# Performance work log

Hardware: AMD Instinct MI355X
Metric: run time of the kernel (lower is better)

## Reference

```python
import jax, jax.numpy as jnp
import numpy as np

N = 100000
E = 1600000
D = 128  # embedding_dim
H = 128  # hidden_channels


def setup_inputs() -> dict:
    key = jax.random.key(0)
    ks = jax.random.split(key, 8)
    x = jax.random.normal(ks[0], (N, D), dtype=jnp.float32)
    edge_index = jax.random.randint(ks[1], (2, E), 0, N, dtype=jnp.int64)
    s = 1.0 / np.sqrt(D)
    W1l = jax.random.uniform(ks[2], (H, D), minval=-s, maxval=s, dtype=jnp.float32)
    W1r = jax.random.uniform(ks[3], (H, D), minval=-s, maxval=s, dtype=jnp.float32)
    b1 = jnp.zeros((H,), dtype=jnp.float32)
    s2 = 1.0 / np.sqrt(H)
    W2l = jax.random.uniform(ks[4], (H, H), minval=-s2, maxval=s2, dtype=jnp.float32)
    W2r = jax.random.uniform(ks[5], (H, H), minval=-s2, maxval=s2, dtype=jnp.float32)
    b2 = jnp.zeros((H,), dtype=jnp.float32)
    return {"x": x, "edge_index": edge_index, "W1l": W1l, "b1": b1, "W1r": W1r,
            "W2l": W2l, "b2": b2, "W2r": W2r}


def _sage_conv(h, src, dst, Wl, b, Wr, n_nodes):
    # mean aggregation of source-node features onto target nodes
    msg = h[src]                                             # [E, F] gather
    agg = jax.ops.segment_sum(msg, dst, num_segments=n_nodes)  # [N, F]
    deg = jax.ops.segment_sum(jnp.ones((src.shape[0],), h.dtype), dst,
                              num_segments=n_nodes)
    mean = agg / jnp.maximum(deg, 1.0)[:, None]
    return mean @ Wl.T + b + h @ Wr.T                        # lin_l(agg) + lin_r(x)


def reference(x, edge_index, W1l, b1, W1r, W2l, b2, W2r):
    src, dst = edge_index[0], edge_index[1]
    n = x.shape[0]
    x1 = jax.nn.relu(_sage_conv(x, src, dst, W1l, b1, W1r, n))
    x2 = jax.nn.relu(_sage_conv(x1, src, dst, W2l, b2, W2r, n))
    return jnp.concatenate((x1[:, :, None], x2[:, :, None]), axis=2)  # [N, H, 2]
```

## Files before the change

kernel.cpp:

```cpp
#include <hip/hip_runtime.h>

typedef unsigned char u8;
typedef unsigned short u16;
typedef unsigned int u32;
typedef unsigned long long u64;
typedef short bf16x8 __attribute__((ext_vector_type(8)));
typedef float f32x4 __attribute__((ext_vector_type(4)));
typedef float f32x2 __attribute__((ext_vector_type(2)));

#define NSB 32
#define MAXW 26
#define CAPL 513
#define CAPW 3072
#define CAPQ 768
#define G1 512
#define CH2 16

static __device__ __forceinline__ float relu(float v) { return v > 0.f ? v : 0.f; }

static __device__ __forceinline__ u16 f2bf(float f) {
  u32 u = __float_as_uint(f);
  u32 r = (u + 0x7FFF + ((u >> 16) & 1)) >> 16;
  return (u16)r;
}
static __device__ __forceinline__ u32 pack2(float a, float b) {
  return (u32)f2bf(a) | ((u32)f2bf(b) << 16);
}

__global__ __launch_bounds__(256) void k_stage(
    const float* __restrict__ w1l, const float* __restrict__ w1r,
    const float* __restrict__ w2l, const float* __restrict__ w2r,
    u16* __restrict__ bfrag,
    const float* __restrict__ x, u16* __restrict__ xb, u8* __restrict__ x8,
    int total8,
    const int* __restrict__ dst, int* __restrict__ Hist1,
    int e, u32 magic, int perBlock, int gPrep, int gF2b) {
  __shared__ int h[NSB];
  int tid = threadIdx.x;
  int b = blockIdx.x;
  if (b < gPrep) {
    int i = b * 256 + tid;
    int ee = i & 7;
    int lane = (i >> 3) & 63;
    int jb = (i >> 9) & 7;
    int ks = (i >> 12) & 7;
    int m = i >> 15;
    int k = ks * 32 + (lane >> 4) * 8 + ee;
    int j = jb * 16 + (lane & 15);
    const float* wl = m ? w2l : w1l;
    const float* wr = m ? w2r : w1r;
    float v = (k < 128) ? wl[j * 128 + k] : wr[j * 128 + (k - 128)];
    bfrag[i] = f2bf(v);
  } else if (b < gPrep + gF2b) {
    int i = (b - gPrep) * 256 + tid;
    if (i < total8) {
      const float4* xp = (const float4*)x;
      float4 a = xp[i * 2];
      float4 bb = xp[i * 2 + 1];
      uint4 o;
      o.x = pack2(a.x, a.y);
      o.y = pack2(a.z, a.w);
      o.z = pack2(bb.x, bb.y);
      o.w = pack2(bb.z, bb.w);
      ((uint4*)xb)[i] = o;
      u32 lo = __builtin_amdgcn_cvt_pk_fp8_f32(a.x, a.y, 0u, false);
      lo = __builtin_amdgcn_cvt_pk_fp8_f32(a.z, a.w, lo, true);
      u32 hi = __builtin_amdgcn_cvt_pk_fp8_f32(bb.x, bb.y, 0u, false);
      hi = __builtin_amdgcn_cvt_pk_fp8_f32(bb.z, bb.w, hi, true);
      uint2 q = {lo, hi};
      ((uint2*)x8)[i] = q;
    }
  } else {
    int hb = b - gPrep - gF2b;
    if (tid < NSB) h[tid] = 0;
    __syncthreads();
    int start = hb * perBlock;
    int end = min(start + perBlock, e);
    for (int i = start + tid; i < end; i += 256) {
      int d = dst[i];
      int sb = (int)(((u64)(u32)d * magic) >> 32);
      atomicAdd(&h[sb], 1);
    }
    __syncthreads();
    if (tid < NSB) Hist1[hb * NSB + tid] = h[tid];
  }
}

__global__ __launch_bounds__(256) void k_offs1(const int* __restrict__ Hist1,
                                               int* __restrict__ Off1,
                                               int* __restrict__ binBase1,
                                               int* __restrict__ binCnt1) {
  __shared__ int tot[NSB], base[NSB];
  int tid = threadIdx.x, lane = tid & 63, wave = tid >> 6;
  for (int b = wave * 8; b < wave * 8 + 8; ++b) {
    int run = 0;
    for (int s = 0; s < G1; s += 64) {
      int v = Hist1[(s + lane) * NSB + b];
      int sum = v;
#pragma unroll
      for (int o = 1; o < 64; o <<= 1) sum += __shfl_xor(sum, o, 64);
      run += sum;
    }
    if (lane == 0) tot[b] = run;
  }
  __syncthreads();
  if (tid == 0) {
    int r = 0;
    for (int b = 0; b < NSB; ++b) {
      base[b] = r;
      binBase1[b] = r;
      binCnt1[b] = tot[b];
      r += tot[b];
    }
  }
  __syncthreads();
  for (int b = wave * 8; b < wave * 8 + 8; ++b) {
    int run = base[b];
    for (int s = 0; s < G1; s += 64) {
      int v = Hist1[(s + lane) * NSB + b];
      int incl = v;
#pragma unroll
      for (int o = 1; o < 64; o <<= 1) {
        int t = __shfl_up(incl, o, 64);
        if (lane >= o) incl += t;
      }
      Off1[(s + lane) * NSB + b] = run + incl - v;
      run += __shfl(incl, 63, 64);
    }
  }
}

__global__ __launch_bounds__(256) void k_scatA(const int* __restrict__ src,
                                               const int* __restrict__ dst,
                                               const int* __restrict__ Off1,
                                               u32* __restrict__ gbinA,
                                               int e, int sbn, u32 magic, int perBlock) {
  __shared__ u32 lbuf[NSB * CAPL];
  __shared__ int lcnt[NSB], myOff[NSB];
  int tid = threadIdx.x, lane = tid & 63, wave = tid >> 6;
  if (tid < NSB) {
    lcnt[tid] = 0;
    myOff[tid] = Off1[blockIdx.x * NSB + tid];
  }
  __syncthreads();
  int start = blockIdx.x * perBlock;
  int end = min(start + perBlock, e);
  for (int base = start; base < end; base += 2048) {
    int bend = min(base + 2048, end);
    for (int i = base + tid; i < bend; i += 256) {
      int d = dst[i];
      int s = src[i];
      int sb = (int)(((u64)(u32)d * magic) >> 32);
      int dl = d - sb * sbn;
      u32 w = (u32)s | ((u32)dl << 17);
      int pos = atomicAdd(&lcnt[sb], 1);
      if (pos < CAPL) lbuf[sb * CAPL + pos] = w;
      else gbinA[myOff[sb] + pos] = w;
    }
    __syncthreads();
    for (int b = wave; b < NSB; b += 4) {
      int cnt = lcnt[b];
      int staged = min(cnt, CAPL);
      int gp = myOff[b];
      for (int off = lane; off < staged; off += 64) gbinA[gp + off] = lbuf[b * CAPL + off];
      if (lane == 0) {
        myOff[b] = gp + cnt;
        lcnt[b] = 0;
      }
    }
    __syncthreads();
  }
}

__global__ __launch_bounds__(256) void k_hist2(const u32* __restrict__ gbinA,
                                               const int* __restrict__ binBase1,
                                               const int* __restrict__ binCnt1,
                                               int* __restrict__ Hist2) {
  __shared__ int h[MAXW];
  int tid = threadIdx.x;
  int sb = blockIdx.x >> 4, ch = blockIdx.x & (CH2 - 1);
  if (tid < MAXW) h[tid] = 0;
  __syncthreads();
  int b0 = binBase1[sb], cnt = binCnt1[sb];
  int per = (cnt + CH2 - 1) / CH2;
  int s = b0 + ch * per, e2 = min(s + per, b0 + cnt);
  for (int i = s + tid; i < e2; i += 256) {
    int wn = (int)(gbinA[i] >> 24);
    atomicAdd(&h[wn], 1);
  }
  __syncthreads();
  if (tid < MAXW) Hist2[blockIdx.x * MAXW + tid] = h[tid];
}

__global__ __launch_bounds__(512) void k_offs2(const int* __restrict__ Hist2,
                                               int* __restrict__ Off2,
                                               int* __restrict__ winBase,
                                               int* __restrict__ winCnt, int wins) {
  __shared__ int tot[NSB * MAXW], baseL[NSB * MAXW];
  int tid = threadIdx.x, lane = tid & 63;
  int nw = NSB * wins;
  for (int wi = tid; wi < nw; wi += 512) {
    int sb = wi / wins, wn = wi - sb * wins;
    int r = 0;
    for (int ch = 0; ch < CH2; ++ch) r += Hist2[(sb * CH2 + ch) * MAXW + wn];
    tot[wi] = r;
  }
  __syncthreads();
  if (tid < 64) {
    int run = 0;
    for (int s = 0; s < nw; s += 64) {
      int idx = s + lane;
      int v = (idx < nw) ? tot[idx] : 0;
      int incl = v;
#pragma unroll
      for (int o = 1; o < 64; o <<= 1) {
        int t = __shfl_up(incl, o, 64);
        if (lane >= o) incl += t;
      }
      if (idx < nw) {
        baseL[idx] = run + incl - v;
        winBase[idx] = run + incl - v;
        winCnt[idx] = v;
      }
      run += __shfl(incl, 63, 64);
    }
  }
  __syncthreads();
  for (int wi = tid; wi < nw; wi += 512) {
    int sb = wi / wins, wn = wi - sb * wins;
    int r = baseL[wi];
    for (int ch = 0; ch < CH2; ++ch) {
      Off2[(sb * CH2 + ch) * MAXW + wn] = r;
      r += Hist2[(sb * CH2 + ch) * MAXW + wn];
    }
  }
}

__global__ __launch_bounds__(256) void k_scatB(const u32* __restrict__ gbinA,
                                               const int* __restrict__ binBase1,
                                               const int* __restrict__ binCnt1,
                                               const int* __restrict__ Off2,
                                               u32* __restrict__ gbin2, int wins) {
  __shared__ u32 lbuf[MAXW * CAPL];
  __shared__ int lcnt[MAXW], myOff[MAXW];
  int tid = threadIdx.x, lane = tid & 63, wave = tid >> 6;
  int sb = blockIdx.x >> 4, ch = blockIdx.x & (CH2 - 1);
  if (tid < MAXW) {
    lcnt[tid] = 0;
    myOff[tid] = Off2[blockIdx.x * MAXW + tid];
  }
  __syncthreads();
  int b0 = binBase1[sb], cnt = binCnt1[sb];
  int per = (cnt + CH2 - 1) / CH2;
  int s = b0 + ch * per, e2 = min(s + per, b0 + cnt);
  for (int base = s; base < e2; base += 2048) {
    int bend = min(base + 2048, e2);
    for (int i = base + tid; i < bend; i += 256) {
      u32 w = gbinA[i];
      int wn = (int)(w >> 24);
      u32 w2 = w & 0x00FFFFFFu;
      int pos = atomicAdd(&lcnt[wn], 1);
      if (pos < CAPL) lbuf[wn * CAPL + pos] = w2;
      else gbin2[myOff[wn] + pos] = w2;
    }
    __syncthreads();
    for (int b = wave; b < wins; b += 4) {
      int c = lcnt[b];
      int staged = min(c, CAPL);
      int gp = myOff[b];
      for (int off = lane; off < staged; off += 64) gbin2[gp + off] = lbuf[b * CAPL + off];
      if (lane == 0) {
        myOff[b] = gp + c;
        lcnt[b] = 0;
      }
    }
    __syncthreads();
  }
}

__global__ __launch_bounds__(256) void k_sort3(const u32* __restrict__ gbin2,
                                               const int* __restrict__ winBase,
                                               const int* __restrict__ winCnt,
                                               u32* __restrict__ gbin3,
                                               int* __restrict__ winOffs) {
  __shared__ int cnt[128], offs[128], cur[128];
  int widx = blockIdx.x, tid = threadIdx.x;
  int wstart = winBase[widx];
  int wcnt = min(winCnt[widx], CAPW);
  if (tid < 128) cnt[tid] = 0;
  __syncthreads();
  for (int i = tid; i < wcnt; i += 256) atomicAdd(&cnt[gbin2[wstart + i] >> 17], 1);
  __syncthreads();
  if (tid < 64) {
    int lane = tid;
    int c0 = cnt[lane * 2], c1 = cnt[lane * 2 + 1];
    int p = c0 + c1, incl = p;
#pragma unroll
    for (int o = 1; o < 64; o <<= 1) {
      int t = __shfl_up(incl, o, 64);
      if (lane >= o) incl += t;
    }
    offs[lane * 2] = incl - p;
    offs[lane * 2 + 1] = incl - c1;
  }
  __syncthreads();
  if (tid < 128) {
    cur[tid] = offs[tid];
    winOffs[(size_t)widx * 128 + tid] = offs[tid];
  }
  __syncthreads();
  for (int i = tid; i < wcnt; i += 256) {
    u32 w = gbin2[wstart + i];
    int pos = atomicAdd(&cur[w >> 17], 1);
    gbin3[wstart + pos] = w & 0x1FFFFu;
  }
}

__global__ __launch_bounds__(256, 8) void k_agg(
    const u8* __restrict__ h8,
    const u32* __restrict__ gbin3,
    const int* __restrict__ winBase, const int* __restrict__ winCnt,
    const int* __restrict__ winOffs, u32* __restrict__ mean,
    int n, int sbn, int wins) {
  __shared__ u32 elist[CAPQ];
  __shared__ int offs[33];
  int tid = threadIdx.x, lane = tid & 63, wid = tid >> 6;
  int widx = blockIdx.x >> 2, quarter = blockIdx.x & 3;
  int sb = widx / wins, win = widx - sb * wins;
  int winNodeBase = sb * sbn + win * 128;
  int rowsTot = min(min(128, sbn - win * 128), n - winNodeBase);
  int rowsQ = min(max(rowsTot - quarter * 32, 0), 32);
  int nodeBase = winNodeBase + quarter * 32;
  int wstart = winBase[widx];
  int wcnt = min(winCnt[widx], CAPW);
  if (tid <= 32) {
    int r = quarter * 32 + tid;
    offs[tid] = (r >= 128) ? wcnt : min(winOffs[(size_t)widx * 128 + r], wcnt);
  }
  __syncthreads();
  int s0 = offs[0];
  int cnt = min(offs[32] - s0, CAPQ);
  for (int i = tid; i < cnt; i += 256) elist[i] = gbin3[wstart + s0 + i];
  __syncthreads();

  int grp = lane >> 4, l16 = lane & 15;
  const uint2* hp = (const uint2*)h8 + l16;
#pragma unroll 1
  for (int rp = 0; rp < 2; ++rp) {
    int r = wid * 8 + rp * 4 + grp;
    int s = offs[r] - s0;
    int c = min(offs[r + 1] - s0, cnt) - s;
    if (c < 0) c = 0;
    f32x2 A0 = {0.f, 0.f}, A1 = {0.f, 0.f}, A2 = {0.f, 0.f}, A3 = {0.f, 0.f};
    uint2 v0 = {0u, 0u}, v1 = {0u, 0u}, v2 = {0u, 0u}, v3 = {0u, 0u};
    if (0 < c) v0 = hp[(size_t)elist[s + 0] * 16];
    if (1 < c) v1 = hp[(size_t)elist[s + 1] * 16];
    if (2 < c) v2 = hp[(size_t)elist[s + 2] * 16];
    if (3 < c) v3 = hp[(size_t)elist[s + 3] * 16];
#pragma unroll 1
    for (int t = 4; t < c + 4; t += 4) {
      uint2 n0 = {0u, 0u}, n1 = {0u, 0u}, n2 = {0u, 0u}, n3 = {0u, 0u};
      if (t + 0 < c) n0 = hp[(size_t)elist[s + t + 0] * 16];
      if (t + 1 < c) n1 = hp[(size_t)elist[s + t + 1] * 16];
      if (t + 2 < c) n2 = hp[(size_t)elist[s + t + 2] * 16];
      if (t + 3 < c) n3 = hp[(size_t)elist[s + t + 3] * 16];
      A0 += __builtin_amdgcn_cvt_pk_f32_fp8(v0.x, false);
      A1 += __builtin_amdgcn_cvt_pk_f32_fp8(v0.x, true);
      A2 += __builtin_amdgcn_cvt_pk_f32_fp8(v0.y, false);
      A3 += __builtin_amdgcn_cvt_pk_f32_fp8(v0.y, true);
      A0 += __builtin_amdgcn_cvt_pk_f32_fp8(v1.x, false);
      A1 += __builtin_amdgcn_cvt_pk_f32_fp8(v1.x, true);
      A2 += __builtin_amdgcn_cvt_pk_f32_fp8(v1.y, false);
      A3 += __builtin_amdgcn_cvt_pk_f32_fp8(v1.y, true);
      A0 += __builtin_amdgcn_cvt_pk_f32_fp8(v2.x, false);
      A1 += __builtin_amdgcn_cvt_pk_f32_fp8(v2.x, true);
      A2 += __builtin_amdgcn_cvt_pk_f32_fp8(v2.y, false);
      A3 += __builtin_amdgcn_cvt_pk_f32_fp8(v2.y, true);
      A0 += __builtin_amdgcn_cvt_pk_f32_fp8(v3.x, false);
      A1 += __builtin_amdgcn_cvt_pk_f32_fp8(v3.x, true);
      A2 += __builtin_amdgcn_cvt_pk_f32_fp8(v3.y, false);
      A3 += __builtin_amdgcn_cvt_pk_f32_fp8(v3.y, true);
      v0 = n0; v1 = n1; v2 = n2; v3 = n3;
    }
    A0 += __builtin_amdgcn_cvt_pk_f32_fp8(v0.x, false);
    A1 += __builtin_amdgcn_cvt_pk_f32_fp8(v0.x, true);
    A2 += __builtin_amdgcn_cvt_pk_f32_fp8(v0.y, false);
    A3 += __builtin_amdgcn_cvt_pk_f32_fp8(v0.y, true);
    A0 += __builtin_amdgcn_cvt_pk_f32_fp8(v1.x, false);
    A1 += __builtin_amdgcn_cvt_pk_f32_fp8(v1.x, true);
    A2 += __builtin_amdgcn_cvt_pk_f32_fp8(v1.y, false);
    A3 += __builtin_amdgcn_cvt_pk_f32_fp8(v1.y, true);
    A0 += __builtin_amdgcn_cvt_pk_f32_fp8(v2.x, false);
    A1 += __builtin_amdgcn_cvt_pk_f32_fp8(v2.x, true);
    A2 += __builtin_amdgcn_cvt_pk_f32_fp8(v2.y, false);
    A3 += __builtin_amdgcn_cvt_pk_f32_fp8(v2.y, true);
    A0 += __builtin_amdgcn_cvt_pk_f32_fp8(v3.x, false);
    A1 += __builtin_amdgcn_cvt_pk_f32_fp8(v3.x, true);
    A2 += __builtin_amdgcn_cvt_pk_f32_fp8(v3.y, false);
    A3 += __builtin_amdgcn_cvt_pk_f32_fp8(v3.y, true);
    if (r < rowsQ) {
      float inv = 1.f / (float)(c > 0 ? c : 1);
      uint4 o;
      o.x = pack2(A0.x * inv, A0.y * inv);
      o.y = pack2(A1.x * inv, A1.y * inv);
      o.z = pack2(A2.x * inv, A2.y * inv);
      o.w = pack2(A3.x * inv, A3.y * inv);
      *(uint4*)(mean + (size_t)(nodeBase + r) * 64 + l16 * 4) = o;
    }
  }
}

template <int MODE>
__global__ __launch_bounds__(512) void k_gemm(
    const u32* __restrict__ Am, const u32* __restrict__ Ax,
    const u16* __restrict__ Bfrag, const float* __restrict__ bias,
    u16* __restrict__ x1out, u8* __restrict__ x8out,
    float* __restrict__ out, int n) {
  __shared__ u16 lA[128 * 256];

  int tid = threadIdx.x, lane = tid & 63, wid = tid >> 6;
  int l15 = lane & 15, lhi = lane >> 4;
  int wr = wid >> 1, wc = wid & 1;
  int r0 = blockIdx.x * 128;

#pragma unroll
  for (int it = 0; it < 8; ++it) {
    int i = tid + it * 512;
    int row = i >> 5, c = i & 31;
    int gr = r0 + row;
    uint4 v = {0u, 0u, 0u, 0u};
    if (gr < n)
      v = (c < 16) ? ((const uint4*)(Am + (size_t)gr * 64))[c]
                   : ((const uint4*)(Ax + (size_t)gr * 64))[c - 16];
    int byteoff = (row * 512 + c * 16) ^ ((row & 7) << 4);
    *(uint4*)((char*)lA + byteoff) = v;
  }

  float bs[4];
#pragma unroll
  for (int nj = 0; nj < 4; ++nj) bs[nj] = bias[wc * 64 + nj * 16 + l15];

  __syncthreads();

  f32x4 acc[2][4];
#pragma unroll
  for (int mi = 0; mi < 2; ++mi)
#pragma unroll
    for (int nj = 0; nj < 4; ++nj) acc[mi][nj] = (f32x4){0.f, 0.f, 0.f, 0.f};

#pragma unroll
  for (int ks = 0; ks < 8; ++ks) {
    bf16x8 af[2], bfr[4];
#pragma unroll
    for (int mi = 0; mi < 2; ++mi) {
      int row = wr * 32 + mi * 16 + l15;
      int byteoff = (row * 512 + ks * 64 + lhi * 16) ^ ((row & 7) << 4);
      af[mi] = *(const bf16x8*)((const char*)lA + byteoff);
    }
#pragma unroll
    for (int nj = 0; nj < 4; ++nj) {
      int jb = wc * 4 + nj;
      bfr[nj] = *(const bf16x8*)(Bfrag + ((ks * 8 + jb) * 64 + lane) * 8);
    }
#pragma unroll
    for (int mi = 0; mi < 2; ++mi)
#pragma unroll
      for (int nj = 0; nj < 4; ++nj)
        acc[mi][nj] = __builtin_amdgcn_mfma_f32_16x16x32_bf16(af[mi], bfr[nj],
                                                              acc[mi][nj], 0, 0, 0);
  }

#pragma unroll
  for (int mi = 0; mi < 2; ++mi) {
#pragma unroll
    for (int r = 0; r < 4; ++r) {
      int rloc = wr * 32 + mi * 16 + lhi * 4 + r;
      int row = r0 + rloc;
      if (row < n) {
#pragma unroll
        for (int nj = 0; nj < 4; ++nj) {
          int col = wc * 64 + nj * 16 + l15;
          float v = relu(acc[mi][nj][r] + bs[nj]);
          if (MODE == 0) {
            x1out[(size_t)row * 128 + col] = f2bf(v);
            u32 pk = __builtin_amdgcn_cvt_pk_fp8_f32(v, v, 0u, false);
            x8out[(size_t)row * 128 + col] = (u8)(pk & 0xFF);
          } else {
            int xoff = (rloc * 512 + 256 + col * 2) ^ ((rloc & 7) << 4);
            u16 x1u = *(const u16*)((const char*)lA + xoff);
            float2 o = {__uint_as_float((u32)x1u << 16), v};
            *(float2*)&out[((size_t)row * 128 + col) * 2] = o;
          }
        }
      }
    }
  }
}

extern "C" void kernel_launch(void* const* d_in, const int* in_sizes, int n_in,
                              void* d_out, int out_size, void* d_ws, size_t ws_size,
                              hipStream_t stream) {
  const float* x = (const float*)d_in[0];
  const int* ei = (const int*)d_in[1];
  const float* w1l = (const float*)d_in[2];
  const float* b1 = (const float*)d_in[3];
  const float* w1r = (const float*)d_in[4];
  const float* w2l = (const float*)d_in[5];
  const float* b2 = (const float*)d_in[6];
  const float* w2r = (const float*)d_in[7];
  float* out = (float*)d_out;

  int n = in_sizes[0] / 128;
  int e = in_sizes[1] / 2;
  const int* src = ei;
  const int* dst = ei + e;

  int sbn = (n + NSB - 1) / NSB;
  int wins = (sbn + 127) / 128;
  u32 magic = (u32)((0x100000000ULL + sbn - 1) / (u64)sbn);

  char* ws = (char*)d_ws;
  size_t off = 0;
  auto alloc = [&](size_t bytes) {
    void* p = ws + off;
    off += (bytes + 255) & ~(size_t)255;
    return p;
  };
  u16* bfrag = (u16*)alloc(65536 * sizeof(u16));
  int* Hist1 = (int*)alloc((size_t)G1 * NSB * 4);
  int* Off1 = (int*)alloc((size_t)G1 * NSB * 4);
  int* binBase1 = (int*)alloc(NSB * 4);
  int* binCnt1 = (int*)alloc(NSB * 4);
  int* Hist2 = (int*)alloc((size_t)NSB * CH2 * MAXW * 4);
  int* Off2 = (int*)alloc((size_t)NSB * CH2 * MAXW * 4);
  int* winBase = (int*)alloc((size_t)NSB * wins * 4);
  int* winCnt = (int*)alloc((size_t)NSB * wins * 4);
  int* winOffs = (int*)alloc((size_t)NSB * wins * 128 * 4);
  u32* gbinA = (u32*)alloc((size_t)e * 4 + 256);
  u32* gbin2 = (u32*)alloc((size_t)e * 4 + 256);
  u16* xb = (u16*)alloc((size_t)n * 128 * sizeof(u16));
  u16* x1b = (u16*)alloc((size_t)n * 128 * sizeof(u16));
  u16* meanb = (u16*)alloc((size_t)n * 128 * sizeof(u16));
  u8* x8 = (u8*)alloc((size_t)n * 128);
  u8* x18 = (u8*)alloc((size_t)n * 128);
  u32* gbin3 = gbinA;
  (void)ws_size;
  (void)n_in;
  (void)out_size;

  int perBlock = (e + G1 - 1) / G1;
  int total8 = n * 128 / 8;
  int gPrep = 256;
  int gF2b = (total8 + 255) / 256;

  k_stage<<<gPrep + gF2b + G1, 256, 0, stream>>>(
      w1l, w1r, w2l, w2r, bfrag, x, xb, x8, total8, dst, Hist1, e, magic,
      perBlock, gPrep, gF2b);
  k_offs1<<<1, 256, 0, stream>>>(Hist1, Off1, binBase1, binCnt1);
  k_scatA<<<G1, 256, 0, stream>>>(src, dst, Off1, gbinA, e, sbn, magic, perBlock);
  k_hist2<<<NSB * CH2, 256, 0, stream>>>(gbinA, binBase1, binCnt1, Hist2);
  k_offs2<<<1, 512, 0, stream>>>(Hist2, Off2, winBase, winCnt, wins);
  k_scatB<<<NSB * CH2, 256, 0, stream>>>(gbinA, binBase1, binCnt1, Off2, gbin2, wins);
  int gW = NSB * wins;
  k_sort3<<<gW, 256, 0, stream>>>(gbin2, winBase, winCnt, gbin3, winOffs);

  int gGemm = (n + 127) / 128;
  k_agg<<<gW * 4, 256, 0, stream>>>(x8, gbin3, winBase, winCnt, winOffs,
                                    (u32*)meanb, n, sbn, wins);
  k_gemm<0><<<gGemm, 512, 0, stream>>>((const u32*)meanb, (const u32*)xb, bfrag, b1,
                                       x1b, x18, nullptr, n);
  k_agg<<<gW * 4, 256, 0, stream>>>(x18, gbin3, winBase, winCnt, winOffs,
                                    (u32*)meanb, n, sbn, wins);
  k_gemm<1><<<gGemm, 512, 0, stream>>>((const u32*)meanb, (const u32*)x1b,
                                       bfrag + 32768, b2, nullptr, nullptr, out, n);
}
```

Baseline: 229.0 us.

## Replace window-level two-pass sort with direct per-node counting sort within superbins

The second and third partitioning passes (per-window scatter, then per-window sort by node) are merged into one counting sort keyed directly by node index within each superbin. It uses a per-node shared-memory histogram, a per-superbin scan kernel that writes node offsets, and a single scatter straight into the final CSR-like order. The aggregation kernel now reads global per-node offsets instead of window-relative ones. This drops one full pass over the edge list and the intermediate buffer, and removes the per-window capacity clamps. In exchange it uses large shared-memory histograms, writes scattered global output with no local staging, and relies on the superbin node count staying below SBMAX.

New measurement: 241.5 us. +5.5%, slower.

```diff
diff --git a/kernel.cpp b/kernel.cpp
--- a/kernel.cpp
+++ b/kernel.cpp
@@ -9,12 +9,11 @@
 typedef float f32x2 __attribute__((ext_vector_type(2)));
 
 #define NSB 32
-#define MAXW 26
 #define CAPL 513
-#define CAPW 3072
 #define CAPQ 768
 #define G1 512
 #define CH2 16
+#define SBMAX 3584
 
 static __device__ __forceinline__ float relu(float v) { return v > 0.f ? v : 0.f; }
 
@@ -172,156 +171,105 @@
   }
 }
 
-__global__ __launch_bounds__(256) void k_hist2(const u32* __restrict__ gbinA,
-                                               const int* __restrict__ binBase1,
-                                               const int* __restrict__ binCnt1,
-                                               int* __restrict__ Hist2) {
-  __shared__ int h[MAXW];
+__global__ __launch_bounds__(256) void k_hist2b(const u32* __restrict__ gbinA,
+                                                const int* __restrict__ binBase1,
+                                                const int* __restrict__ binCnt1,
+                                                int* __restrict__ Hist2,
+                                                int sbn, int pad) {
+  __shared__ int h[SBMAX];
   int tid = threadIdx.x;
   int sb = blockIdx.x >> 4, ch = blockIdx.x & (CH2 - 1);
-  if (tid < MAXW) h[tid] = 0;
+  for (int i = tid; i < sbn; i += 256) h[i] = 0;
   __syncthreads();
   int b0 = binBase1[sb], cnt = binCnt1[sb];
   int per = (cnt + CH2 - 1) / CH2;
   int s = b0 + ch * per, e2 = min(s + per, b0 + cnt);
   for (int i = s + tid; i < e2; i += 256) {
-    int wn = (int)(gbinA[i] >> 24);
-    atomicAdd(&h[wn], 1);
-  }
-  __syncthreads();
-  if (tid < MAXW) Hist2[blockIdx.x * MAXW + tid] = h[tid];
-}
-
-__global__ __launch_bounds__(512) void k_offs2(const int* __restrict__ Hist2,
-                                               int* __restrict__ Off2,
-                                               int* __restrict__ winBase,
-                                               int* __restrict__ winCnt, int wins) {
-  __shared__ int tot[NSB * MAXW], baseL[NSB * MAXW];
-  int tid = threadIdx.x, lane = tid & 63;
-  int nw = NSB * wins;
-  for (int wi = tid; wi < nw; wi += 512) {
-    int sb = wi / wins, wn = wi - sb * wins;
-    int r = 0;
-    for (int ch = 0; ch < CH2; ++ch) r += Hist2[(sb * CH2 + ch) * MAXW + wn];
-    tot[wi] = r;
-  }
-  __syncthreads();
-  if (tid < 64) {
-    int run = 0;
-    for (int s = 0; s < nw; s += 64) {
-      int idx = s + lane;
-      int v = (idx < nw) ? tot[idx] : 0;
-      int incl = v;
-#pragma unroll
-      for (int o = 1; o < 64; o <<= 1) {
-        int t = __shfl_up(incl, o, 64);
-        if (lane >= o) incl += t;
+    atomicAdd(&h[gbinA[i] >> 17], 1);
+  }
+  __syncthreads();
+  int* out = Hist2 + (size_t)(sb * CH2 + ch) * pad;
+  for (int i = tid; i < sbn; i += 256) out[i] = h[i];
+}
+
+__global__ __launch_bounds__(256) void k_offs2b(const int* __restrict__ Hist2,
+                                                int* __restrict__ Off2,
+                                                int* __restrict__ nodeOffs,
+                                                const int* __restrict__ binBase1,
+                                                const int* __restrict__ binCnt1,
+                                                int sbn, int pad, int nsb) {
+  __shared__ int wtot[4];
+  __shared__ int carry;
+  int sb = blockIdx.x;
+  int tid = threadIdx.x, lane = tid & 63, wv = tid >> 6;
+  if (tid == 0) carry = binBase1[sb];
+  __syncthreads();
+  for (int ph = 0; ph < sbn; ph += 256) {
+    int dl = ph + tid;
+    bool valid = dl < sbn;
+    int c[CH2];
+    int total = 0;
+#pragma unroll
+    for (int ch = 0; ch < CH2; ++ch) {
+      c[ch] = valid ? Hist2[(size_t)(sb * CH2 + ch) * pad + dl] : 0;
+      total += c[ch];
+    }
+    int incl = total;
+#pragma unroll
+    for (int o = 1; o < 64; o <<= 1) {
+      int t = __shfl_up(incl, o, 64);
+      if (lane >= o) incl += t;
+    }
+    if (lane == 63) wtot[wv] = incl;
+    __syncthreads();
+    int wbase = 0;
+    for (int w2 = 0; w2 < wv; ++w2) wbase += wtot[w2];
+    int excl = carry + wbase + incl - total;
+    if (valid) {
+      nodeOffs[(size_t)sb * sbn + dl] = excl;
+      int run = excl;
+#pragma unroll
+      for (int ch = 0; ch < CH2; ++ch) {
+        Off2[(size_t)(sb * CH2 + ch) * pad + dl] = run;
+        run += c[ch];
       }
-      if (idx < nw) {
-        baseL[idx] = run + incl - v;
-        winBase[idx] = run + incl - v;
-        winCnt[idx] = v;
-      }
-      run += __shfl(incl, 63, 64);
-    }
-  }
-  __syncthreads();
-  for (int wi = tid; wi < nw; wi += 512) {
-    int sb = wi / wins, wn = wi - sb * wins;
-    int r = baseL[wi];
-    for (int ch = 0; ch < CH2; ++ch) {
-      Off2[(sb * CH2 + ch) * MAXW + wn] = r;
-      r += Hist2[(sb * CH2 + ch) * MAXW + wn];
-    }
-  }
-}
-
-__global__ __launch_bounds__(256) void k_scatB(const u32* __restrict__ gbinA,
-                                               const int* __restrict__ binBase1,
-                                               const int* __restrict__ binCnt1,
-                                               const int* __restrict__ Off2,
-                                               u32* __restrict__ gbin2, int wins) {
-  __shared__ u32 lbuf[MAXW * CAPL];
-  __shared__ int lcnt[MAXW], myOff[MAXW];
-  int tid = threadIdx.x, lane = tid & 63, wave = tid >> 6;
+    }
+    int newc = excl + total;
+    __syncthreads();
+    if (tid == 255) carry = newc;
+    __syncthreads();
+  }
+  if (sb == nsb - 1 && tid == 0)
+    nodeOffs[(size_t)nsb * sbn] = binBase1[sb] + binCnt1[sb];
+}
+
+__global__ __launch_bounds__(256) void k_scatB2(const u32* __restrict__ gbinA,
+                                                const int* __restrict__ binBase1,
+                                                const int* __restrict__ binCnt1,
+                                                const int* __restrict__ Off2,
+                                                u32* __restrict__ gbin3,
+                                                int sbn, int pad) {
+  __shared__ int cur[SBMAX];
+  int tid = threadIdx.x;
   int sb = blockIdx.x >> 4, ch = blockIdx.x & (CH2 - 1);
-  if (tid < MAXW) {
-    lcnt[tid] = 0;
-    myOff[tid] = Off2[blockIdx.x * MAXW + tid];
-  }
+  const int* offp = Off2 + (size_t)(sb * CH2 + ch) * pad;
+  for (int i = tid; i < sbn; i += 256) cur[i] = offp[i];
   __syncthreads();
   int b0 = binBase1[sb], cnt = binCnt1[sb];
   int per = (cnt + CH2 - 1) / CH2;
   int s = b0 + ch * per, e2 = min(s + per, b0 + cnt);
-  for (int base = s; base < e2; base += 2048) {
-    int bend = min(base + 2048, e2);
-    for (int i = base + tid; i < bend; i += 256) {
-      u32 w = gbinA[i];
-      int wn = (int)(w >> 24);
-      u32 w2 = w & 0x00FFFFFFu;
-      int pos = atomicAdd(&lcnt[wn], 1);
-      if (pos < CAPL) lbuf[wn * CAPL + pos] = w2;
-      else gbin2[myOff[wn] + pos] = w2;
-    }
-    __syncthreads();
-    for (int b = wave; b < wins; b += 4) {
-      int c = lcnt[b];
-      int staged = min(c, CAPL);
-      int gp = myOff[b];
-      for (int off = lane; off < staged; off += 64) gbin2[gp + off] = lbuf[b * CAPL + off];
-      if (lane == 0) {
-        myOff[b] = gp + c;
-        lcnt[b] = 0;
-      }
-    }
-    __syncthreads();
-  }
-}
-
-__global__ __launch_bounds__(256) void k_sort3(const u32* __restrict__ gbin2,
-                                               const int* __restrict__ winBase,
-                                               const int* __restrict__ winCnt,
-                                               u32* __restrict__ gbin3,
-                                               int* __restrict__ winOffs) {
-  __shared__ int cnt[128], offs[128], cur[128];
-  int widx = blockIdx.x, tid = threadIdx.x;
-  int wstart = winBase[widx];
-  int wcnt = min(winCnt[widx], CAPW);
-  if (tid < 128) cnt[tid] = 0;
-  __syncthreads();
-  for (int i = tid; i < wcnt; i += 256) atomicAdd(&cnt[gbin2[wstart + i] >> 17], 1);
-  __syncthreads();
-  if (tid < 64) {
-    int lane = tid;
-    int c0 = cnt[lane * 2], c1 = cnt[lane * 2 + 1];
-    int p = c0 + c1, incl = p;
-#pragma unroll
-    for (int o = 1; o < 64; o <<= 1) {
-      int t = __shfl_up(incl, o, 64);
-      if (lane >= o) incl += t;
-    }
-    offs[lane * 2] = incl - p;
-    offs[lane * 2 + 1] = incl - c1;
-  }
-  __syncthreads();
-  if (tid < 128) {
-    cur[tid] = offs[tid];
-    winOffs[(size_t)widx * 128 + tid] = offs[tid];
-  }
-  __syncthreads();
-  for (int i = tid; i < wcnt; i += 256) {
-    u32 w = gbin2[wstart + i];
+  for (int i = s + tid; i < e2; i += 256) {
+    u32 w = gbinA[i];
     int pos = atomicAdd(&cur[w >> 17], 1);
-    gbin3[wstart + pos] = w & 0x1FFFFu;
+    gbin3[pos] = w & 0x1FFFFu;
   }
 }
 
 __global__ __launch_bounds__(256, 8) void k_agg(
     const u8* __restrict__ h8,
     const u32* __restrict__ gbin3,
-    const int* __restrict__ winBase, const int* __restrict__ winCnt,
-    const int* __restrict__ winOffs, u32* __restrict__ mean,
-    int n, int sbn, int wins) {
+    const int* __restrict__ nodeOffs, u32* __restrict__ mean,
+    int n, int sbn, int wins, int totScan) {
   __shared__ u32 elist[CAPQ];
   __shared__ int offs[33];
   int tid = threadIdx.x, lane = tid & 63, wid = tid >> 6;
@@ -331,16 +279,16 @@
   int rowsTot = min(min(128, sbn - win * 128), n - winNodeBase);
   int rowsQ = min(max(rowsTot - quarter * 32, 0), 32);
   int nodeBase = winNodeBase + quarter * 32;
-  int wstart = winBase[widx];
-  int wcnt = min(winCnt[widx], CAPW);
+  if (rowsQ <= 0) return;
   if (tid <= 32) {
-    int r = quarter * 32 + tid;
-    offs[tid] = (r >= 128) ? wcnt : min(winOffs[(size_t)widx * 128 + r], wcnt);
+    int gi = nodeBase + tid;
+    if (gi > totScan) gi = totScan;
+    offs[tid] = nodeOffs[gi];
   }
   __syncthreads();
   int s0 = offs[0];
-  int cnt = min(offs[32] - s0, CAPQ);
-  for (int i = tid; i < cnt; i += 256) elist[i] = gbin3[wstart + s0 + i];
+  int cnt = min(max(offs[32] - s0, 0), CAPQ);
+  for (int i = tid; i < cnt; i += 256) elist[i] = gbin3[s0 + i];
   __syncthreads();
 
   int grp = lane >> 4, l16 = lane & 15;
@@ -517,6 +465,7 @@
 
   int sbn = (n + NSB - 1) / NSB;
   int wins = (sbn + 127) / 128;
+  int pad = (sbn + 63) & ~63;
   u32 magic = (u32)((0x100000000ULL + sbn - 1) / (u64)sbn);
 
   char* ws = (char*)d_ws;
@@ -531,19 +480,16 @@
   int* Off1 = (int*)alloc((size_t)G1 * NSB * 4);
   int* binBase1 = (int*)alloc(NSB * 4);
   int* binCnt1 = (int*)alloc(NSB * 4);
-  int* Hist2 = (int*)alloc((size_t)NSB * CH2 * MAXW * 4);
-  int* Off2 = (int*)alloc((size_t)NSB * CH2 * MAXW * 4);
-  int* winBase = (int*)alloc((size_t)NSB * wins * 4);
-  int* winCnt = (int*)alloc((size_t)NSB * wins * 4);
-  int* winOffs = (int*)alloc((size_t)NSB * wins * 128 * 4);
+  int* Hist2 = (int*)alloc((size_t)NSB * CH2 * pad * 4);
+  int* Off2 = (int*)alloc((size_t)NSB * CH2 * pad * 4);
+  int* nodeOffs = (int*)alloc(((size_t)NSB * sbn + 64) * 4);
   u32* gbinA = (u32*)alloc((size_t)e * 4 + 256);
-  u32* gbin2 = (u32*)alloc((size_t)e * 4 + 256);
+  u32* gbin3 = (u32*)alloc((size_t)e * 4 + 256);
   u16* xb = (u16*)alloc((size_t)n * 128 * sizeof(u16));
   u16* x1b = (u16*)alloc((size_t)n * 128 * sizeof(u16));
   u16* meanb = (u16*)alloc((size_t)n * 128 * sizeof(u16));
   u8* x8 = (u8*)alloc((size_t)n * 128);
   u8* x18 = (u8*)alloc((size_t)n * 128);
-  u32* gbin3 = gbinA;
   (void)ws_size;
   (void)n_in;
   (void)out_size;
@@ -552,25 +498,27 @@
   int total8 = n * 128 / 8;
   int gPrep = 256;
   int gF2b = (total8 + 255) / 256;
+  int totScan = NSB * sbn;
 
   k_stage<<<gPrep + gF2b + G1, 256, 0, stream>>>(
       w1l, w1r, w2l, w2r, bfrag, x, xb, x8, total8, dst, Hist1, e, magic,
       perBlock, gPrep, gF2b);
   k_offs1<<<1, 256, 0, stream>>>(Hist1, Off1, binBase1, binCnt1);
   k_scatA<<<G1, 256, 0, stream>>>(src, dst, Off1, gbinA, e, sbn, magic, perBlock);
-  k_hist2<<<NSB * CH2, 256, 0, stream>>>(gbinA, binBase1, binCnt1, Hist2);
-  k_offs2<<<1, 512, 0, stream>>>(Hist2, Off2, winBase, winCnt, wins);
-  k_scatB<<<NSB * CH2, 256, 0, stream>>>(gbinA, binBase1, binCnt1, Off2, gbin2, wins);
+  k_hist2b<<<NSB * CH2, 256, 0, stream>>>(gbinA, binBase1, binCnt1, Hist2, sbn, pad);
+  k_offs2b<<<NSB, 256, 0, stream>>>(Hist2, Off2, nodeOffs, binBase1, binCnt1,
+                                    sbn, pad, NSB);
+  k_scatB2<<<NSB * CH2, 256, 0, stream>>>(gbinA, binBase1, binCnt1, Off2, gbin3,
+                                          sbn, pad);
+
   int gW = NSB * wins;
-  k_sort3<<<gW, 256, 0, stream>>>(gbin2, winBase, winCnt, gbin3, winOffs);
-
   int gGemm = (n + 127) / 128;
-  k_agg<<<gW * 4, 256, 0, stream>>>(x8, gbin3, winBase, winCnt, winOffs,
-                                    (u32*)meanb, n, sbn, wins);
+  k_agg<<<gW * 4, 256, 0, stream>>>(x8, gbin3, nodeOffs, (u32*)meanb, n, sbn,
+                                    wins, totScan);
   k_gemm<0><<<gGemm, 512, 0, stream>>>((const u32*)meanb, (const u32*)xb, bfrag, b1,
                                        x1b, x18, nullptr, n);
-  k_agg<<<gW * 4, 256, 0, stream>>>(x18, gbin3, winBase, winCnt, winOffs,
-                                    (u32*)meanb, n, sbn, wins);
+  k_agg<<<gW * 4, 256, 0, stream>>>(x18, gbin3, nodeOffs, (u32*)meanb, n, sbn,
+                                    wins, totScan);
   k_gemm<1><<<gGemm, 512, 0, stream>>>((const u32*)meanb, (const u32*)x1b,
                                        bfrag + 32768, b2, nullptr, nullptr, out, n);
 }
```
